# Performance work log

Measured on AMD Instinct MI355X. Metric: run time of the kernel, lower is better.

The kernel has to match this reference:

```python
import jax, jax.numpy as jnp
import numpy as np

B, N, TD, SD, BD, K, M, TOPK, H = 8, 1024, 5120, 2048, 1024, 16, 4, 2, 8
HD = SD // H  # 256


def _ln(x, g, b, eps=1e-5):
    m = jnp.mean(x, -1, keepdims=True)
    v = jnp.mean((x - m) ** 2, -1, keepdims=True)
    return (x - m) * jax.lax.rsqrt(v + eps) * g + b


def _adapter(h, dw, db, uw, ub, lg, lb, q, wq, bq, wk, bk, wv, bv, ow, ob, pg, pb):
    # bottleneck trunk: down -> GELU -> up -> LN (dropout = identity in eval)
    x = jax.nn.gelu(h @ dw + db, approximate=False)          # [B,N,BD]
    x = _ln(x @ uw + ub, lg, lb)                             # [B,N,SD]
    Bb = x.shape[0]
    # cross-attention: learnable queries [K,SD] attend over x
    qp = (q @ wq + bq).reshape(K, H, HD).transpose(1, 0, 2)                      # [H,K,HD]
    kp = (x @ wk + bk).reshape(Bb, -1, H, HD).transpose(0, 2, 1, 3)              # [B,H,N,HD]
    vp = (x @ wv + bv).reshape(Bb, -1, H, HD).transpose(0, 2, 1, 3)              # [B,H,N,HD]
    att = jax.nn.softmax(jnp.einsum('hkd,bhnd->bhkn', qp, kp) * (1.0 / np.sqrt(HD)), axis=-1)
    ctx = jnp.einsum('bhkn,bhnd->bhkd', att, vp).transpose(0, 2, 1, 3).reshape(Bb, K, SD)
    ctx = ctx @ ow + ob
    return _ln(ctx + q[None], pg, pb)                        # residual with queries


def setup_inputs():
    key = jax.random.key(0)
    it = iter(jax.random.split(key, 40))
    def nrm(shape, s=0.02):
        return jax.random.normal(next(it), shape, jnp.float32) * s
    inp = {'h_teacher': jax.random.normal(next(it), (B, N, TD), jnp.float32)}
    for pre, lead in (('g_', ()), ('s_', (M,))):
        inp[pre + 'dw'] = nrm(lead + (TD, BD)); inp[pre + 'db'] = jnp.zeros(lead + (BD,), jnp.float32)
        inp[pre + 'uw'] = nrm(lead + (BD, SD)); inp[pre + 'ub'] = jnp.zeros(lead + (SD,), jnp.float32)
        inp[pre + 'lg'] = jnp.ones(lead + (SD,), jnp.float32); inp[pre + 'lb'] = jnp.zeros(lead + (SD,), jnp.float32)
        inp[pre + 'q'] = nrm(lead + (K, SD))
        for nm in ('wq', 'wk', 'wv', 'ow'):
            inp[pre + nm] = nrm(lead + (SD, SD))
        for nm in ('bq', 'bk', 'bv', 'ob'):
            inp[pre + nm] = jnp.zeros(lead + (SD,), jnp.float32)
        inp[pre + 'pg'] = jnp.ones(lead + (SD,), jnp.float32); inp[pre + 'pb'] = jnp.zeros(lead + (SD,), jnp.float32)
    inp['r_w1'] = nrm((TD, 512)); inp['r_b1'] = jnp.zeros((512,), jnp.float32)
    inp['r_w2'] = nrm((512, M)); inp['r_b2'] = jnp.zeros((M,), jnp.float32)
    return inp


def reference(h_teacher, g_dw, g_db, g_uw, g_ub, g_lg, g_lb, g_q, g_wq, g_bq, g_wk, g_bk, g_wv, g_bv, g_ow, g_ob, g_pg, g_pb, s_dw, s_db, s_uw, s_ub, s_lg, s_lb, s_q, s_wq, s_bq, s_wk, s_bk, s_wv, s_bv, s_ow, s_ob, s_pg, s_pb, r_w1, r_b1, r_w2, r_b2):
    # generalized adapter (always on)
    c_g = _adapter(h_teacher, g_dw, g_db, g_uw, g_ub, g_lg, g_lb, g_q, g_wq, g_bq, g_wk, g_bk, g_wv, g_bv, g_ow, g_ob, g_pg, g_pb)
    # all specialized experts computed densely (as the torch module does), then gathered
    c_spec = jax.vmap(lambda dw, db, uw, ub, lg, lb, q, wq, bq, wk, bk, wv, bv, ow, ob, pg, pb:
                      _adapter(h_teacher, dw, db, uw, ub, lg, lb, q, wq, bq, wk, bk, wv, bv, ow, ob, pg, pb))(
        s_dw, s_db, s_uw, s_ub, s_lg, s_lb, s_q, s_wq, s_bq, s_wk, s_bk, s_wv, s_bv, s_ow, s_ob, s_pg, s_pb)  # [M,B,K,SD]
    cs = jnp.transpose(c_spec, (1, 0, 2, 3))                 # [B,M,K,SD]
    # router on mean-pooled teacher summary (eval: no noise)
    pooled = jnp.mean(h_teacher, axis=1)                     # [B,TD]
    logits = jax.nn.gelu(pooled @ r_w1 + r_b1, approximate=False) @ r_w2 + r_b2
    probs = jax.nn.softmax(logits, axis=-1)                  # [B,M]
    w, idx = jax.lax.top_k(probs, TOPK)                      # [B,TOPK]
    w = w / (jnp.sum(w, -1, keepdims=True) + 1e-8)
    sel = cs[jnp.arange(cs.shape[0])[:, None], idx]          # [B,TOPK,K,SD]
    c_s = jnp.sum(sel * w[:, :, None, None], axis=1)         # [B,K,SD]
    c_agg = jnp.concatenate([c_g, c_s], axis=1)              # [B,2K,SD]
    return c_agg, probs
```

## Files before the change

### kernel.cpp

```cpp
#include <hip/hip_runtime.h>
#include <hip/hip_bf16.h>

#define B_   8
#define N_   1024
#define TD_  5120
#define SD_  2048
#define BD_  1024
#define K_   16
#define H_   8

typedef unsigned short u16;
typedef __attribute__((ext_vector_type(8))) short bf16x8;
typedef __attribute__((ext_vector_type(4))) float f32x4;
typedef __attribute__((ext_vector_type(8))) u16 u16x8;

__device__ __forceinline__ float bf2f(u16 u) {
    union { unsigned int i; float f; } x; x.i = ((unsigned)u) << 16; return x.f;
}
__device__ __forceinline__ u16 f2bf(float f) {
    union { float f; unsigned int i; } x; x.f = f;
    unsigned int i = x.i;
    return (u16)((i + 0x7fffu + ((i >> 16) & 1u)) >> 16);
}
__device__ __forceinline__ float gelu_exact(float v) {
    return 0.5f * v * (1.0f + erff(v * 0.70710678118654752f));
}
__device__ __forceinline__ void gload_lds16(const void* g, void* l) {
    __builtin_amdgcn_global_load_lds(
        (const __attribute__((address_space(1))) unsigned int*)g,
        (__attribute__((address_space(3))) unsigned int*)l, 16, 0, 0);
}

struct Ptr5 { const float* p[5]; };
struct Ptr40 { const float* p[8][5]; };

template<int EPI, int AMODE>
__global__ __launch_bounds__(256, 4)
void gemm128(const u16* __restrict__ Abase,
             const u16* __restrict__ Bbase, long bStride,
             const float* __restrict__ biasBase, int biasStride,
             u16* __restrict__ Cbase, int ldc, long cStride, int Kd,
             const int* __restrict__ units_a, const int* __restrict__ units_b)
{
    __shared__ char lds[32768];
    const int u = blockIdx.z;
    const int ua = units_a[u];
    const int ub = (AMODE == 0) ? units_b[u] : u;
    const u16* A  = Abase + (size_t)ub * 1024 * Kd;
    const u16* Bt = Bbase + (size_t)ua * bStride;
    const float* bias = biasBase + (size_t)ua * biasStride;
    u16* C = Cbase + (size_t)u * cStride;

    const int tid  = threadIdx.x;
    const int wave = tid >> 6, lane = tid & 63;
    const int wm = wave >> 1, wn = wave & 1;
    const int row0 = blockIdx.x * 128, col0 = blockIdx.y * 128;

    const int srow = tid >> 3;
    const int scol = ((tid & 7) ^ (srow & 7)) << 3;
    const char* aSrc = (const char*)(A  + (size_t)(row0 + srow) * Kd + scol);
    const char* bSrc = (const char*)(Bt + (size_t)(col0 + srow) * Kd + scol);
    const int ldsW = wave * 1024;

    const int fr = lane & 15, fq = lane >> 4;
    const int kl  = fq << 4;
    const int swz = (fr & 7) << 4;

    f32x4 acc[4][4] = {};

#define LDA_(mf, kk) (*(const bf16x8*)(lds + \
    (wm*64 + (mf)*16 + fr)*128 + ((((kk)*64) + kl) ^ swz)))
#define LDB_(nf, kk) (*(const bf16x8*)(lds + 16384 + \
    (wn*64 + (nf)*16 + fr)*128 + ((((kk)*64) + kl) ^ swz)))

    const int nt = Kd >> 6;
    for (int T = 0; T < nt; ++T) {
        const size_t kb = (size_t)T << 7;
#pragma unroll
        for (int l = 0; l < 4; ++l)
            gload_lds16(aSrc + (size_t)(l*32)*Kd*2 + kb, lds + l*4096 + ldsW);
#pragma unroll
        for (int l = 0; l < 4; ++l)
            gload_lds16(bSrc + (size_t)(l*32)*Kd*2 + kb, lds + 16384 + l*4096 + ldsW);
        asm volatile("s_waitcnt vmcnt(0)" ::: "memory");
        __syncthreads();
#pragma unroll
        for (int kk = 0; kk < 2; ++kk) {
            bf16x8 aF[4], bF[4];
#pragma unroll
            for (int i = 0; i < 4; ++i) aF[i] = LDA_(i, kk);
#pragma unroll
            for (int n = 0; n < 4; ++n) bF[n] = LDB_(n, kk);
#pragma unroll
            for (int i = 0; i < 4; ++i)
#pragma unroll
                for (int n = 0; n < 4; ++n)
                    acc[i][n] = __builtin_amdgcn_mfma_f32_16x16x32_bf16(
                        aF[i], bF[n], acc[i][n], 0, 0, 0);
        }
        __syncthreads();
    }

#undef LDA_
#undef LDB_

#pragma unroll
    for (int mf = 0; mf < 4; ++mf)
#pragma unroll
        for (int nf = 0; nf < 4; ++nf) {
            const int col = col0 + wn*64 + nf*16 + fr;
            const float bv = bias[col];
#pragma unroll
            for (int j = 0; j < 4; ++j) {
                const int row = row0 + wm*64 + mf*16 + fq*4 + j;
                float v = acc[mf][nf][j] + bv;
                if (EPI == 1) v = gelu_exact(v);
                C[(size_t)row*ldc + col] = f2bf(v);
            }
        }
}

__global__ void cvt_bf16_flat(const float* __restrict__ in, u16* __restrict__ out, long n8) {
    long i = (long)blockIdx.x * blockDim.x + threadIdx.x;
    const long stride = (long)gridDim.x * blockDim.x;
    for (; i < n8; i += stride) {
        const f32x4* p = (const f32x4*)in + i*2;
        f32x4 a = p[0], b = p[1];
        u16x8 o;
        o[0]=f2bf(a[0]); o[1]=f2bf(a[1]); o[2]=f2bf(a[2]); o[3]=f2bf(a[3]);
        o[4]=f2bf(b[0]); o[5]=f2bf(b[1]); o[6]=f2bf(b[2]); o[7]=f2bf(b[3]);
        ((u16x8*)out)[i] = o;
    }
}

__global__ __launch_bounds__(256)
void cvt_transpose(const float* __restrict__ W, u16* __restrict__ Wt, int Kd, int Nd) {
    __shared__ float t[64][65];
    const int k0 = blockIdx.x * 64, n0 = blockIdx.y * 64;
    const int tid = threadIdx.x;
#pragma unroll
    for (int i = 0; i < 4; ++i) {
        int ch = tid + i*256;
        int r = ch >> 4, c4 = (ch & 15) << 2;
        f32x4 v = *(const f32x4*)(W + (size_t)(k0 + r)*Nd + n0 + c4);
        t[r][c4] = v[0]; t[r][c4+1] = v[1]; t[r][c4+2] = v[2]; t[r][c4+3] = v[3];
    }
    __syncthreads();
#pragma unroll
    for (int i = 0; i < 2; ++i) {
        int ch = tid + i*256;
        int nr = ch >> 3, c8 = (ch & 7) << 3;
        u16x8 o;
#pragma unroll
        for (int j = 0; j < 8; ++j) o[j] = f2bf(t[c8 + j][nr]);
        *(u16x8*)(Wt + (size_t)(n0 + nr)*Kd + k0 + c8) = o;
    }
}

__global__ __launch_bounds__(256)
void ln_rows_u(u16* __restrict__ X, const float* __restrict__ gslab,
               const float* __restrict__ bslab, const int* __restrict__ units_a) {
    const int row = blockIdx.x, tid = threadIdx.x;
    const int ua = units_a[row >> 10];
    const float* g  = gslab + (size_t)ua*SD_;
    const float* bt = bslab + (size_t)ua*SD_;
    u16* rp = X + (size_t)row*SD_;
    const u16x8 v = ((const u16x8*)rp)[tid];
    float f[8]; float s = 0.f, s2 = 0.f;
#pragma unroll
    for (int j = 0; j < 8; ++j) { f[j] = bf2f(v[j]); s += f[j]; s2 += f[j]*f[j]; }
    __shared__ float sa[4], sb[4];
#pragma unroll
    for (int o = 32; o > 0; o >>= 1) { s += __shfl_down(s, o); s2 += __shfl_down(s2, o); }
    if ((tid & 63) == 0) { sa[tid >> 6] = s; sb[tid >> 6] = s2; }
    __syncthreads();
    s = sa[0]+sa[1]+sa[2]+sa[3]; s2 = sb[0]+sb[1]+sb[2]+sb[3];
    const float mean = s * (1.0f/SD_);
    const float inv  = rsqrtf(s2 * (1.0f/SD_) - mean*mean + 1e-5f);
    const int c0 = tid*8;
    u16x8 o;
#pragma unroll
    for (int j = 0; j < 8; ++j) o[j] = f2bf((f[j]-mean)*inv*g[c0+j] + bt[c0+j]);
    ((u16x8*)rp)[tid] = o;
}

__global__ __launch_bounds__(256)
void qp_part(Ptr5 q, Ptr5 wq, float* __restrict__ Sp) {
    __shared__ float qL[16][256];
    const int a = blockIdx.y, ks = blockIdx.z;
    const int c = blockIdx.x*256 + threadIdx.x;
    const int t = threadIdx.x;
    const float* Q = q.p[a];
    for (int i = t; i < 16*256; i += 256)
        qL[i >> 8][i & 255] = Q[(size_t)(i >> 8)*SD_ + ks*256 + (i & 255)];
    __syncthreads();
    const float* W = wq.p[a] + (size_t)(ks*256)*SD_ + c;
    float acc[16] = {};
    for (int i = 0; i < 256; i += 4) {
        const float w0 = W[(size_t)i*SD_];
        const float w1 = W[(size_t)(i+1)*SD_];
        const float w2 = W[(size_t)(i+2)*SD_];
        const float w3 = W[(size_t)(i+3)*SD_];
#pragma unroll
        for (int k = 0; k < 16; ++k) {
            f32x4 q4 = *(const f32x4*)&qL[k][i];
            acc[k] += q4[0]*w0 + q4[1]*w1 + q4[2]*w2 + q4[3]*w3;
        }
    }
#pragma unroll
    for (int k = 0; k < 16; ++k)
        Sp[((size_t)(a*8 + ks)*16 + k)*SD_ + c] = acc[k];
}

__global__ void qp_reduce(const float* __restrict__ Sp, Ptr5 bq, float* __restrict__ qp) {
    const int idx = blockIdx.x*256 + threadIdx.x;
    const int a = idx >> 15, k = (idx >> 11) & 15, c = idx & 2047;
    float s = bq.p[a][c];
#pragma unroll
    for (int ks = 0; ks < 8; ++ks)
        s += Sp[((size_t)(a*8 + ks)*16 + k)*SD_ + c];
    qp[idx] = s;
}

__global__ __launch_bounds__(256)
void scores_sm(const u16* __restrict__ Kb, const float* __restrict__ qp,
               const int* __restrict__ units_a, float* __restrict__ P)
{
    __shared__ float sL[16][1024];
    __shared__ float qL[16][256];
    __shared__ float red[8];
    const int u = blockIdx.x >> 3, hh = blockIdx.x & 7;
    const int ua = units_a[u];
    const int t = threadIdx.x;
    for (int i = t; i < 16*256; i += 256)
        qL[i >> 8][i & 255] = qp[(size_t)(ua*16 + (i >> 8))*SD_ + hh*256 + (i & 255)];
    __syncthreads();
    const u16* Ku = Kb + (size_t)u*1024*SD_ + hh*256;
#pragma unroll
    for (int j = 0; j < 4; ++j) {
        const int n = t + j*256;
        const u16* kr = Ku + (size_t)n*SD_;
        float acc[16] = {};
        for (int d0 = 0; d0 < 256; d0 += 8) {
            u16x8 kv8 = *(const u16x8*)(kr + d0);
            float kf[8];
#pragma unroll
            for (int e = 0; e < 8; ++e) kf[e] = bf2f(kv8[e]);
#pragma unroll
            for (int k = 0; k < 16; ++k) {
                f32x4 q0 = *(const f32x4*)&qL[k][d0];
                f32x4 q1 = *(const f32x4*)&qL[k][d0+4];
                acc[k] += q0[0]*kf[0] + q0[1]*kf[1] + q0[2]*kf[2] + q0[3]*kf[3]
                        + q1[0]*kf[4] + q1[1]*kf[5] + q1[2]*kf[6] + q1[3]*kf[7];
            }
        }
#pragma unroll
        for (int k = 0; k < 16; ++k) sL[k][n] = acc[k] * 0.0625f;
    }
    __syncthreads();
    const int lane = t & 63, wv = t >> 6;
    for (int k = 0; k < 16; ++k) {
        float v0 = sL[k][t], v1 = sL[k][t+256], v2 = sL[k][t+512], v3 = sL[k][t+768];
        float mx = fmaxf(fmaxf(v0,v1), fmaxf(v2,v3));
#pragma unroll
        for (int o = 1; o < 64; o <<= 1) mx = fmaxf(mx, __shfl_xor(mx, o));
        if (lane == 0) red[wv] = mx;
        __syncthreads();
        mx = fmaxf(fmaxf(red[0],red[1]), fmaxf(red[2],red[3]));
        float e0 = expf(v0-mx), e1 = expf(v1-mx), e2 = expf(v2-mx), e3 = expf(v3-mx);
        float s = e0+e1+e2+e3;
#pragma unroll
        for (int o = 1; o < 64; o <<= 1) s += __shfl_xor(s, o);
        if (lane == 0) red[4+wv] = s;
        __syncthreads();
        s = red[4]+red[5]+red[6]+red[7];
        const float inv = 1.0f/s;
        float* Pr = P + ((size_t)(u*8+hh)*16 + k)*1024;
        Pr[t]=e0*inv; Pr[t+256]=e1*inv; Pr[t+512]=e2*inv; Pr[t+768]=e3*inv;
        __syncthreads();
    }
}

__global__ __launch_bounds__(256)
void ctx_u(const u16* __restrict__ Vb, const float* __restrict__ P,
           u16* __restrict__ ctxb)
{
    __shared__ float pL[16][1024];
    const int u = blockIdx.x >> 3, hh = blockIdx.x & 7;
    const int t = threadIdx.x;
    const float* Pu = P + (size_t)(u*8+hh)*16*1024;
    for (int i = t; i < 16*1024/4; i += 256)
        ((f32x4*)&pL[0][0])[i] = ((const f32x4*)Pu)[i];
    __syncthreads();
    const u16* Vu = Vb + (size_t)u*1024*SD_ + hh*256 + t;
    float acc[16] = {};
    for (int n = 0; n < 1024; n += 4) {
        float vv0 = bf2f(Vu[(size_t)n*SD_]);
        float vv1 = bf2f(Vu[(size_t)(n+1)*SD_]);
        float vv2 = bf2f(Vu[(size_t)(n+2)*SD_]);
        float vv3 = bf2f(Vu[(size_t)(n+3)*SD_]);
#pragma unroll
        for (int k = 0; k < 16; ++k) {
            f32x4 p4 = *(const f32x4*)&pL[k][n];
            acc[k] += p4[0]*vv0 + p4[1]*vv1 + p4[2]*vv2 + p4[3]*vv3;
        }
    }
#pragma unroll
    for (int k = 0; k < 16; ++k)
        ctxb[(size_t)u*16*SD_ + k*SD_ + hh*256 + t] = f2bf(acc[k]);
}

__global__ __launch_bounds__(256)
void gemm_ow(const u16* __restrict__ ctxb, const u16* __restrict__ Bslab,
             const float* __restrict__ biasSlab, const int* __restrict__ units_a,
             float* __restrict__ ctx2)
{
    const int u = blockIdx.y, ua = units_a[u];
    const int wave = threadIdx.x >> 6, lane = threadIdx.x & 63;
    const int col0 = blockIdx.x*256 + wave*64;
    const u16* A  = ctxb + (size_t)u*16*SD_;
    const u16* Bt = Bslab + (size_t)ua*SD_*SD_;
    const int fr = lane & 15, fk8 = (lane >> 4) << 3;
    f32x4 acc[4] = {};
    for (int k0 = 0; k0 < SD_; k0 += 32) {
        bf16x8 af = *(const bf16x8*)(A + (size_t)fr*SD_ + k0 + fk8);
#pragma unroll
        for (int n = 0; n < 4; ++n) {
            bf16x8 bf8 = *(const bf16x8*)(Bt + (size_t)(col0 + n*16 + fr)*SD_ + k0 + fk8);
            acc[n] = __builtin_amdgcn_mfma_f32_16x16x32_bf16(af, bf8, acc[n], 0, 0, 0);
        }
    }
    const int fq = lane >> 4;
#pragma unroll
    for (int n = 0; n < 4; ++n)
#pragma unroll
        for (int j = 0; j < 4; ++j) {
            const int row = fq*4 + j, col = col0 + n*16 + fr;
            ctx2[(size_t)u*16*SD_ + (size_t)row*SD_ + col] = acc[n][j] + biasSlab[ua*SD_ + col];
        }
}

__global__ __launch_bounds__(256)
void ln_post_u(const float* __restrict__ ctx2, const float* __restrict__ qslab,
               const float* __restrict__ pgs, const float* __restrict__ pbs,
               const int* __restrict__ units_a, const int* __restrict__ units_b,
               float* __restrict__ out, float* __restrict__ cspec)
{
    const int k = blockIdx.x, u = blockIdx.y, tid = threadIdx.x;
    const int ua = units_a[u];
    const float* ip = ctx2 + ((size_t)u*16 + k)*SD_;
    const float* qr = qslab + ((size_t)ua*16 + k)*SD_;
    const float* g  = pgs + (size_t)ua*SD_;
    const float* bt = pbs + (size_t)ua*SD_;
    float f[8]; float s = 0.f, s2 = 0.f;
#pragma unroll
    for (int j = 0; j < 8; ++j) {
        const int c = tid + j*256;
        f[j] = ip[c] + qr[c];
        s += f[j]; s2 += f[j]*f[j];
    }
    __shared__ float sa[4], sb[4];
#pragma unroll
    for (int o = 32; o > 0; o >>= 1) { s += __shfl_down(s, o); s2 += __shfl_down(s2, o); }
    if ((tid & 63) == 0) { sa[tid >> 6] = s; sb[tid >> 6] = s2; }
    __syncthreads();
    s = sa[0]+sa[1]+sa[2]+sa[3]; s2 = sb[0]+sb[1]+sb[2]+sb[3];
    const float mean = s * (1.0f/SD_);
    const float inv  = rsqrtf(s2 * (1.0f/SD_) - mean*mean + 1e-5f);
    float* op = (u < 8) ? out + ((size_t)units_b[u]*32 + k)*SD_
                        : cspec + ((size_t)(u-8)*16 + k)*SD_;
#pragma unroll
    for (int j = 0; j < 8; ++j) { const int c = tid + j*256; op[c] = (f[j]-mean)*inv*g[c] + bt[c]; }
}

__global__ __launch_bounds__(256)
void pool_part(const float* __restrict__ h, float* __restrict__ pp) {
    const int c = blockIdx.x*256 + threadIdx.x;
    const int b = blockIdx.y, ns = blockIdx.z;
    const float* p = h + ((size_t)b*N_ + ns*256)*TD_ + c;
    float s = 0.f;
    for (int n = 0; n < 256; ++n) s += p[(size_t)n*TD_];
    pp[(size_t)ns*8*TD_ + (size_t)b*TD_ + c] = s;
}
__global__ void pool_reduce(const float* __restrict__ pp, float* __restrict__ pooled) {
    const int idx = blockIdx.x*256 + threadIdx.x;
    const float s = pp[idx] + pp[idx + 8*TD_] + pp[idx + 16*TD_] + pp[idx + 24*TD_];
    pooled[idx] = s * (1.0f/N_);
}

__global__ __launch_bounds__(256)
void rmlp_part(const float* __restrict__ pooled, const float* __restrict__ w1,
               float* __restrict__ rp) {
    const int c = blockIdx.x*256 + threadIdx.x;
    const int b = blockIdx.y, is = blockIdx.z;
    const float* pr = pooled + b*TD_ + is*512;
    const float* W = w1 + (size_t)(is*512)*512 + c;
    float s = 0.f;
    for (int i = 0; i < 512; ++i) s += pr[i] * W[(size_t)i*512];
    rp[(b*10 + is)*512 + c] = s;
}
__global__ void rmlp_reduce(const float* __restrict__ rp, const float* __restrict__ b1,
                            float* __restrict__ hid) {
    const int idx = blockIdx.x*256 + threadIdx.x;
    const int b = idx >> 9, c = idx & 511;
    float s = b1[c];
#pragma unroll
    for (int is = 0; is < 10; ++is) s += rp[(b*10 + is)*512 + c];
    hid[idx] = gelu_exact(s);
}

__global__ void router_final(const float* __restrict__ hid, const float* __restrict__ w2,
                             const float* __restrict__ b2, float* __restrict__ probs,
                             int* __restrict__ widx, float* __restrict__ wval,
                             int* __restrict__ units_a, int* __restrict__ units_b) {
    __shared__ float lg[8][4];
    __shared__ int sw[16];
    const int tid = threadIdx.x;
    if (tid < 32) {
        const int b = tid >> 2, m = tid & 3;
        float s = b2[m];
        const float* hr = hid + b*512;
        for (int i = 0; i < 512; ++i) s += hr[i]*w2[i*4 + m];
        lg[b][m] = s;
    }
    __syncthreads();
    if (tid < 8) {
        const int b = tid;
        const float l0=lg[b][0], l1=lg[b][1], l2=lg[b][2], l3=lg[b][3];
        const float mx = fmaxf(fmaxf(l0,l1),fmaxf(l2,l3));
        const float e0=expf(l0-mx), e1=expf(l1-mx), e2=expf(l2-mx), e3=expf(l3-mx);
        const float s = e0+e1+e2+e3;
        float p[4] = {e0/s, e1/s, e2/s, e3/s};
        probs[b*4+0]=p[0]; probs[b*4+1]=p[1]; probs[b*4+2]=p[2]; probs[b*4+3]=p[3];
        int i0 = 0;
        for (int m = 1; m < 4; ++m) if (p[m] > p[i0]) i0 = m;
        int i1 = -1;
        for (int m = 0; m < 4; ++m) if (m != i0 && (i1 < 0 || p[m] > p[i1])) i1 = m;
        const float w0 = p[i0], w1 = p[i1], ws = w0 + w1 + 1e-8f;
        widx[b*2]=i0; widx[b*2+1]=i1;
        wval[b*2]=w0/ws; wval[b*2+1]=w1/ws;
        sw[b*2]=i0; sw[b*2+1]=i1;
    }
    __syncthreads();
    if (tid < 24) {
        units_a[tid] = (tid < 8) ? 0 : sw[tid-8] + 1;
        units_b[tid] = (tid < 8) ? tid : ((tid-8) >> 1);
    }
}

__global__ void combine_k(const float* __restrict__ cspec, const int* __restrict__ widx,
                          const float* __restrict__ wval, float* __restrict__ out) {
    const int i = blockIdx.x*256 + threadIdx.x;
    const int c4 = i & 511;
    const int k  = (i >> 9) & 15;
    const int b  = i >> 13;
    const float w0 = wval[b*2], w1 = wval[b*2+1];
    const f32x4 v0 = ((const f32x4*)cspec)[(size_t)((2*b)  *16 + k)*512 + c4];
    const f32x4 v1 = ((const f32x4*)cspec)[(size_t)((2*b+1)*16 + k)*512 + c4];
    ((f32x4*)out)[(size_t)(b*32 + 16 + k)*512 + c4] = v0*w0 + v1*w1;
}

__global__ void pack5(Ptr5 src, float* __restrict__ dst, int len) {
    int i = blockIdx.x*256 + threadIdx.x;
    if (i < 5*len) dst[i] = src.p[i/len][i%len];
}
__global__ void pack_slab8(Ptr40 s, float* __restrict__ dst) {
    int i = blockIdx.x*256 + threadIdx.x;
    int slab = i / 10240, rem = i % 10240;
    dst[i] = s.p[slab][rem / 2048][rem % 2048];
}

extern "C" void kernel_launch(void* const* d_in, const int* in_sizes, int n_in,
                              void* d_out, int out_size, void* d_ws, size_t ws_size,
                              hipStream_t stream) {
    if (ws_size < 300300000ULL) return;

    const float* h = (const float*)d_in[0];
    const float* G[17]; const float* Sx[17];
    for (int i = 0; i < 17; ++i) { G[i] = (const float*)d_in[1+i]; Sx[i] = (const float*)d_in[18+i]; }
    const float* r_w1 = (const float*)d_in[35];
    const float* r_b1 = (const float*)d_in[36];
    const float* r_w2 = (const float*)d_in[37];
    const float* r_b2 = (const float*)d_in[38];

    static const size_t str[17] = {
        (size_t)TD_*BD_, BD_, (size_t)BD_*SD_, SD_, SD_, SD_, (size_t)K_*SD_,
        (size_t)SD_*SD_, (size_t)SD_*SD_, (size_t)SD_*SD_, (size_t)SD_*SD_,
        SD_, SD_, SD_, SD_, SD_, SD_ };
    auto P = [&](int pi, int a) -> const float* {
        return (a == 0) ? G[pi] : Sx[pi] + (size_t)(a-1)*str[pi];
    };

    char* w = (char*)d_ws;
    const size_t R0 = 0, R1 = 100663296, R2 = 201326592, R3 = 251658240, TAIL = 293601280;
    u16*   h_bf  = (u16*)(w + R0);
    u16*   X     = (u16*)(w + R0);
    u16*   wt_dw = (u16*)(w + R1);
    u16*   Kbuf  = (u16*)(w + R1);
    u16*   X1    = (u16*)(w + R2);
    u16*   wt_v  = (u16*)(w + R2);
    u16*   wt_ow = (u16*)(w + R2);
    u16*   wt_uw = (u16*)(w + R3);
    u16*   wt_k  = (u16*)(w + R3);
    u16*   ctxb  = (u16*)(w + R3);
    float* ctx2  = (float*)(w + R3 + 1572864);
    float* cspec = (float*)(w + R3 + 4718592);
    float* Pbuf  = (float*)(w + R3 + 6815744);
    float* qpp   = (float*)(w + R2);
    float* poolp = (float*)(w + R2 + 12582912);
    float* routp = (float*)(w + R2 + 14680064);
    float* qp_all  = (float*)(w + TAIL);
    float* qslab   = (float*)(w + TAIL + 655360);
    float* bias_dw = (float*)(w + TAIL + 1310720);
    float* slab8   = (float*)(w + TAIL + 1331200);
    float* pooled  = (float*)(w + TAIL + 1658880);
    float* hid     = (float*)(w + TAIL + 1822720);
    int*   widx    = (int*)  (w + TAIL + 1839104);
    float* wval    = (float*)(w + TAIL + 1839168);
    int*   units_a = (int*)  (w + TAIL + 1839232);
    int*   units_b = (int*)  (w + TAIL + 1839328);

    float* bias_uw = slab8;
    float* bias_k  = slab8 + 1*5*SD_;
    float* bias_v  = slab8 + 2*5*SD_;
    float* bias_ow = slab8 + 3*5*SD_;
    float* lng     = slab8 + 4*5*SD_;
    float* lnb     = slab8 + 5*5*SD_;
    float* pgs     = slab8 + 6*5*SD_;
    float* pbs     = slab8 + 7*5*SD_;

    float* out = (float*)d_out;

    cvt_bf16_flat<<<2048, 256, 0, stream>>>(h, h_bf, (long)((size_t)B_*N_*TD_/8));
    pool_part<<<dim3(20, 8, 4), 256, 0, stream>>>(h, poolp);
    pool_reduce<<<160, 256, 0, stream>>>(poolp, pooled);
    rmlp_part<<<dim3(2, 8, 10), 256, 0, stream>>>(pooled, r_w1, routp);
    rmlp_reduce<<<16, 256, 0, stream>>>(routp, r_b1, hid);
    router_final<<<1, 64, 0, stream>>>(hid, r_w2, r_b2, out + 524288, widx, wval, units_a, units_b);

    Ptr5 q5, wq5, bq5, db5;
    for (int a = 0; a < 5; ++a) { q5.p[a]=P(6,a); wq5.p[a]=P(7,a); bq5.p[a]=P(11,a); db5.p[a]=P(1,a); }
    qp_part<<<dim3(8, 5, 8), 256, 0, stream>>>(q5, wq5, qpp);
    qp_reduce<<<640, 256, 0, stream>>>(qpp, bq5, qp_all);
    pack5<<<20, 256, 0, stream>>>(db5, bias_dw, BD_);
    pack5<<<640, 256, 0, stream>>>(q5, qslab, 16*SD_);
    Ptr40 s8;
    static const int slab_pi[8] = {3, 12, 13, 14, 4, 5, 15, 16};
    for (int si = 0; si < 8; ++si)
        for (int a = 0; a < 5; ++a) s8.p[si][a] = P(slab_pi[si], a);
    pack_slab8<<<320, 256, 0, stream>>>(s8, slab8);

    for (int a = 0; a < 5; ++a) {
        cvt_transpose<<<dim3(TD_/64, BD_/64), 256, 0, stream>>>(P(0,a), wt_dw + (size_t)a*BD_*TD_, TD_, BD_);
        cvt_transpose<<<dim3(BD_/64, SD_/64), 256, 0, stream>>>(P(2,a), wt_uw + (size_t)a*SD_*BD_, BD_, SD_);
    }

    gemm128<1, 0><<<dim3(8, 8, 24), 256, 0, stream>>>(
        h_bf, wt_dw, (long)BD_*TD_, bias_dw, BD_, X1, BD_, (long)1024*BD_, TD_, units_a, units_b);

    gemm128<0, 1><<<dim3(8, 16, 24), 256, 0, stream>>>(
        X1, wt_uw, (long)SD_*BD_, bias_uw, SD_, X, SD_, (long)1024*SD_, BD_, units_a, units_b);

    ln_rows_u<<<24*1024, 256, 0, stream>>>(X, lng, lnb, units_a);

    for (int a = 0; a < 5; ++a) {
        cvt_transpose<<<dim3(SD_/64, SD_/64), 256, 0, stream>>>(P(8,a), wt_k + (size_t)a*SD_*SD_, SD_, SD_);
        cvt_transpose<<<dim3(SD_/64, SD_/64), 256, 0, stream>>>(P(9,a), wt_v + (size_t)a*SD_*SD_, SD_, SD_);
    }

    gemm128<0, 1><<<dim3(8, 16, 24), 256, 0, stream>>>(
        X, wt_k, (long)SD_*SD_, bias_k, SD_, Kbuf, SD_, (long)1024*SD_, SD_, units_a, units_b);

    scores_sm<<<24*8, 256, 0, stream>>>(Kbuf, qp_all, units_a, Pbuf);

    gemm128<0, 1><<<dim3(8, 16, 24), 256, 0, stream>>>(
        X, wt_v, (long)SD_*SD_, bias_v, SD_, Kbuf, SD_, (long)1024*SD_, SD_, units_a, units_b);

    for (int a = 0; a < 5; ++a)
        cvt_transpose<<<dim3(SD_/64, SD_/64), 256, 0, stream>>>(P(10,a), wt_ow + (size_t)a*SD_*SD_, SD_, SD_);

    ctx_u<<<24*8, 256, 0, stream>>>(Kbuf, Pbuf, ctxb);

    gemm_ow<<<dim3(8, 24), 256, 0, stream>>>(ctxb, wt_ow, bias_ow, units_a, ctx2);

    ln_post_u<<<dim3(16, 24), 256, 0, stream>>>(ctx2, qslab, pgs, pbs, units_a, units_b, out, cspec);
    combine_k<<<256, 256, 0, stream>>>(cspec, widx, wval, out);
}
```

Measured before the change: 1.475 ms.

## Replace 128x128 GEMM with 256x256 tile, 4-stage pipelined LDS prefetch kernel

The bf16 MFMA GEMM now computes 256x256 output tiles with 512 threads. Each wave owns 128x64 of the output, so every LDS fragment feeds more MFMAs. The K loop uses 32-wide steps and a 4-buffer ring in 128KB of LDS, issuing global-to-LDS loads three tiles ahead instead of waiting on vmcnt(0) every step. It also raises MFMA priority with setprio. This targets load latency stalls and low operand reuse in the four dominant GEMMs. The cost is one block per CU, fewer blocks overall (e.g. 384 for the down projection), and more accumulator registers.

```diff
diff --git a/kernel.cpp b/kernel.cpp
--- a/kernel.cpp
+++ b/kernel.cpp
@@ -35,14 +35,14 @@
 struct Ptr40 { const float* p[8][5]; };
 
 template<int EPI, int AMODE>
-__global__ __launch_bounds__(256, 4)
-void gemm128(const u16* __restrict__ Abase,
-             const u16* __restrict__ Bbase, long bStride,
-             const float* __restrict__ biasBase, int biasStride,
-             u16* __restrict__ Cbase, int ldc, long cStride, int Kd,
-             const int* __restrict__ units_a, const int* __restrict__ units_b)
+__global__ __launch_bounds__(512, 1)
+void gemm256d(const u16* __restrict__ Abase,
+              const u16* __restrict__ Bbase, long bStride,
+              const float* __restrict__ biasBase, int biasStride,
+              u16* __restrict__ Cbase, int ldc, long cStride, int Kd,
+              const int* __restrict__ units_a, const int* __restrict__ units_b)
 {
-    __shared__ char lds[32768];
+    __shared__ char lds[131072];
     const int u = blockIdx.z;
     const int ua = units_a[u];
     const int ub = (AMODE == 0) ? units_b[u] : u;
@@ -53,66 +53,102 @@
 
     const int tid  = threadIdx.x;
     const int wave = tid >> 6, lane = tid & 63;
-    const int wm = wave >> 1, wn = wave & 1;
-    const int row0 = blockIdx.x * 128, col0 = blockIdx.y * 128;
-
-    const int srow = tid >> 3;
-    const int scol = ((tid & 7) ^ (srow & 7)) << 3;
-    const char* aSrc = (const char*)(A  + (size_t)(row0 + srow) * Kd + scol);
-    const char* bSrc = (const char*)(Bt + (size_t)(col0 + srow) * Kd + scol);
+    const int wm = wave >> 2, wn = wave & 3;
+    const int row0 = blockIdx.x * 256, col0 = blockIdx.y * 256;
+    const int fr = lane & 15, fq = lane >> 4;
+
+    long asrc[2], bsrc[2];
+    {
+        const int p = tid & 7;
+#pragma unroll
+        for (int l = 0; l < 2; ++l) {
+            const int line = (tid >> 3) + l*64;
+            const int lg = p ^ (line & 7);
+            const int half = lg >> 2, c = lg & 3;
+            asrc[l] = (long)(row0 + line + 128*half)*Kd*2 + c*16;
+            bsrc[l] = (long)(col0 + line + 128*half)*Kd*2 + c*16;
+        }
+    }
+    const char* aB = (const char*)A;
+    const char* bB = (const char*)Bt;
     const int ldsW = wave * 1024;
 
-    const int fr = lane & 15, fq = lane >> 4;
-    const int kl  = fq << 4;
-    const int swz = (fr & 7) << 4;
-
-    f32x4 acc[4][4] = {};
-
-#define LDA_(mf, kk) (*(const bf16x8*)(lds + \
-    (wm*64 + (mf)*16 + fr)*128 + ((((kk)*64) + kl) ^ swz)))
-#define LDB_(nf, kk) (*(const bf16x8*)(lds + 16384 + \
-    (wn*64 + (nf)*16 + fr)*128 + ((((kk)*64) + kl) ^ swz)))
-
-    const int nt = Kd >> 6;
+    f32x4 acc[8][4] = {};
+    bf16x8 aF[4], bF[4];
+
+#define STAGE_T(kt, sb) do { \
+    const long ko_ = (long)(kt) * 64; \
+    char* db_ = lds + (sb)*32768 + ldsW; \
+    gload_lds16(aB + asrc[0] + ko_, db_); \
+    gload_lds16(aB + asrc[1] + ko_, db_ + 8192); \
+    gload_lds16(bB + bsrc[0] + ko_, db_ + 16384); \
+    gload_lds16(bB + bsrc[1] + ko_, db_ + 24576); } while(0)
+
+#define LDA_(bufp, mf) (*(const bf16x8*)((bufp) + \
+    (((mf)*16 + fr) * 128) + (((wm*4 + fq) ^ (fr & 7)) * 16)))
+#define LDB_(bufp, nf) (*(const bf16x8*)((bufp) + 16384 + \
+    ((((wn & 1)*64) + (nf)*16 + fr) * 128) + ((((wn >> 1)*4 + fq) ^ (fr & 7)) * 16)))
+
+#define FENCE_ asm volatile("" ::: "memory")
+#define BAR_   __builtin_amdgcn_s_barrier()
+#define WAITL_ do { asm volatile("s_waitcnt lgkmcnt(0)" ::: "memory"); \
+                    __builtin_amdgcn_sched_barrier(0); } while(0)
+#define VM8_   asm volatile("s_waitcnt vmcnt(8)" ::: "memory")
+#define MFMA16_(mh) { __builtin_amdgcn_s_setprio(1); \
+    _Pragma("unroll") for (int i_ = 0; i_ < 4; ++i_) { \
+      _Pragma("unroll") for (int n_ = 0; n_ < 4; ++n_) \
+        acc[(mh)*4+i_][n_] = __builtin_amdgcn_mfma_f32_16x16x32_bf16( \
+            aF[i_], bF[n_], acc[(mh)*4+i_][n_], 0, 0, 0); } \
+    __builtin_amdgcn_s_setprio(0); }
+
+    const int nt = Kd >> 5;
+    STAGE_T(0, 0); STAGE_T(1, 1); STAGE_T(2, 2);
+    VM8_;
+    BAR_;
+
+#pragma unroll 4
     for (int T = 0; T < nt; ++T) {
-        const size_t kb = (size_t)T << 7;
-#pragma unroll
-        for (int l = 0; l < 4; ++l)
-            gload_lds16(aSrc + (size_t)(l*32)*Kd*2 + kb, lds + l*4096 + ldsW);
-#pragma unroll
-        for (int l = 0; l < 4; ++l)
-            gload_lds16(bSrc + (size_t)(l*32)*Kd*2 + kb, lds + 16384 + l*4096 + ldsW);
-        asm volatile("s_waitcnt vmcnt(0)" ::: "memory");
-        __syncthreads();
-#pragma unroll
-        for (int kk = 0; kk < 2; ++kk) {
-            bf16x8 aF[4], bF[4];
-#pragma unroll
-            for (int i = 0; i < 4; ++i) aF[i] = LDA_(i, kk);
-#pragma unroll
-            for (int n = 0; n < 4; ++n) bF[n] = LDB_(n, kk);
-#pragma unroll
-            for (int i = 0; i < 4; ++i)
-#pragma unroll
-                for (int n = 0; n < 4; ++n)
-                    acc[i][n] = __builtin_amdgcn_mfma_f32_16x16x32_bf16(
-                        aF[i], bF[n], acc[i][n], 0, 0, 0);
-        }
-        __syncthreads();
-    }
-
+        const int sb = T & 3;
+        const int kt = (T + 3 < nt) ? T + 3 : nt - 1;
+        const char* bufp = lds + sb*32768;
+        FENCE_;
+#pragma unroll
+        for (int n = 0; n < 4; ++n) bF[n] = LDB_(bufp, n);
+#pragma unroll
+        for (int i = 0; i < 4; ++i) aF[i] = LDA_(bufp, i);
+        STAGE_T(kt, (T + 3) & 3);
+        BAR_;
+        WAITL_;
+        MFMA16_(0);
+        BAR_;
+        FENCE_;
+#pragma unroll
+        for (int i = 0; i < 4; ++i) aF[i] = LDA_(bufp, 4 + i);
+        VM8_;
+        BAR_;
+        WAITL_;
+        MFMA16_(1);
+        BAR_;
+    }
+
+#undef STAGE_T
 #undef LDA_
 #undef LDB_
-
-#pragma unroll
-    for (int mf = 0; mf < 4; ++mf)
+#undef FENCE_
+#undef BAR_
+#undef WAITL_
+#undef VM8_
+#undef MFMA16_
+
+#pragma unroll
+    for (int mf = 0; mf < 8; ++mf)
 #pragma unroll
         for (int nf = 0; nf < 4; ++nf) {
             const int col = col0 + wn*64 + nf*16 + fr;
             const float bv = bias[col];
 #pragma unroll
             for (int j = 0; j < 4; ++j) {
-                const int row = row0 + wm*64 + mf*16 + fq*4 + j;
+                const int row = row0 + wm*128 + mf*16 + fq*4 + j;
                 float v = acc[mf][nf][j] + bv;
                 if (EPI == 1) v = gelu_exact(v);
                 C[(size_t)row*ldc + col] = f2bf(v);
@@ -555,10 +591,10 @@
         cvt_transpose<<<dim3(BD_/64, SD_/64), 256, 0, stream>>>(P(2,a), wt_uw + (size_t)a*SD_*BD_, BD_, SD_);
     }
 
-    gemm128<1, 0><<<dim3(8, 8, 24), 256, 0, stream>>>(
+    gemm256d<1, 0><<<dim3(4, 4, 24), 512, 0, stream>>>(
         h_bf, wt_dw, (long)BD_*TD_, bias_dw, BD_, X1, BD_, (long)1024*BD_, TD_, units_a, units_b);
 
-    gemm128<0, 1><<<dim3(8, 16, 24), 256, 0, stream>>>(
+    gemm256d<0, 1><<<dim3(4, 8, 24), 512, 0, stream>>>(
         X1, wt_uw, (long)SD_*BD_, bias_uw, SD_, X, SD_, (long)1024*SD_, BD_, units_a, units_b);
 
     ln_rows_u<<<24*1024, 256, 0, stream>>>(X, lng, lnb, units_a);
@@ -568,12 +604,12 @@
         cvt_transpose<<<dim3(SD_/64, SD_/64), 256, 0, stream>>>(P(9,a), wt_v + (size_t)a*SD_*SD_, SD_, SD_);
     }
 
-    gemm128<0, 1><<<dim3(8, 16, 24), 256, 0, stream>>>(
+    gemm256d<0, 1><<<dim3(4, 8, 24), 512, 0, stream>>>(
         X, wt_k, (long)SD_*SD_, bias_k, SD_, Kbuf, SD_, (long)1024*SD_, SD_, units_a, units_b);
 
     scores_sm<<<24*8, 256, 0, stream>>>(Kbuf, qp_all, units_a, Pbuf);
 
-    gemm128<0, 1><<<dim3(8, 16, 24), 256, 0, stream>>>(
+    gemm256d<0, 1><<<dim3(4, 8, 24), 512, 0, stream>>>(
         X, wt_v, (long)SD_*SD_, bias_v, SD_, Kbuf, SD_, (long)1024*SD_, SD_, units_a, units_b);
 
     for (int a = 0; a < 5; ++a)
```

Measured after the change: 1.518 ms. 1.03x slower.
